# Optimization experiments

Hardware: AMD Instinct MI355X
Metric: run time of the kernel (lower is better)

Reference implementation:

```python
import jax, jax.numpy as jnp
import numpy as np

N = 100000
D_IN = 64
D_HID = 64


def _sage_conv(x, edge_index, Wl, bl, Wr):
    # PyG SAGEConv (mean aggr): out = lin_l(mean_j x_j) + lin_r(x_root)
    src, dst = edge_index[0], edge_index[1]
    n = x.shape[0]
    msg_sum = jax.ops.segment_sum(x[src], dst, num_segments=n)  # [N, d]
    deg = jax.ops.segment_sum(jnp.ones_like(src, dtype=x.dtype), dst, num_segments=n)
    agg = msg_sum / jnp.maximum(deg, 1.0)[:, None]
    return agg @ Wl + bl + x @ Wr


def setup_inputs() -> dict:
    key = jax.random.key(0)
    ks = jax.random.split(key, 8)
    x = jax.random.normal(ks[0], (N, D_IN), dtype=jnp.float32)
    edge_index = jax.random.randint(ks[1], (2, 16 * N), 0, N, dtype=jnp.int64)
    s = 1.0 / np.sqrt(D_IN)
    W1l = jax.random.uniform(ks[2], (D_IN, D_HID), minval=-s, maxval=s, dtype=jnp.float32)
    b1 = jnp.zeros((D_HID,), dtype=jnp.float32)
    W1r = jax.random.uniform(ks[3], (D_IN, D_HID), minval=-s, maxval=s, dtype=jnp.float32)
    s2 = 1.0 / np.sqrt(D_HID)
    W2l = jax.random.uniform(ks[4], (D_HID, D_HID), minval=-s2, maxval=s2, dtype=jnp.float32)
    b2 = jnp.zeros((D_HID,), dtype=jnp.float32)
    W2r = jax.random.uniform(ks[5], (D_HID, D_HID), minval=-s2, maxval=s2, dtype=jnp.float32)
    Wc = jax.random.uniform(ks[6], (D_HID, 2), minval=-s2, maxval=s2, dtype=jnp.float32)
    bc = jax.random.uniform(ks[7], (2,), minval=-s2, maxval=s2, dtype=jnp.float32)
    return {"x": x, "edge_index": edge_index, "W1l": W1l, "b1": b1, "W1r": W1r,
            "W2l": W2l, "b2": b2, "W2r": W2r, "Wc": Wc, "bc": bc}


def reference(x, edge_index, W1l, b1, W1r, W2l, b2, W2r, Wc, bc):
    h = jax.nn.relu(_sage_conv(x, edge_index, W1l, b1, W1r))
    h = _sage_conv(h, edge_index, W2l, b2, W2r)
    return h @ Wc + bc  # [N, 2] logits
```

## Files before the change

kernel.cpp:

```cpp
#include <hip/hip_runtime.h>


#define SCAN_BS 1024
#define BUCKET_BITS 9
#define BUCKET_NODES 512
#define NBUCK_MAX 256
#define EPB 8192
#define STAGE_CAP 10240

__global__ void __launch_bounds__(256) bucket_hist_kernel(const int* __restrict__ dst,
                                                          int* __restrict__ counts,
                                                          int ne, int B, int NB) {
  __shared__ int hist[NBUCK_MAX];
  for (int k = threadIdx.x; k < B; k += 256) hist[k] = 0;
  __syncthreads();
  int base = blockIdx.x * EPB;
#pragma unroll 4
  for (int i = 0; i < EPB / 256; ++i) {
    int e = base + i * 256 + threadIdx.x;
    if (e < ne) atomicAdd(&hist[dst[e] >> BUCKET_BITS], 1);
  }
  __syncthreads();
  for (int k = threadIdx.x; k < B; k += 256) counts[k * NB + blockIdx.x] = hist[k];
}

__device__ __forceinline__ int block_scan_inclusive_1024(int v, int* wsums) {
  int lane = threadIdx.x & 63;
  int wid = threadIdx.x >> 6;
  int s = v;
#pragma unroll
  for (int off = 1; off < 64; off <<= 1) {
    int t = __shfl_up(s, off);
    if (lane >= off) s += t;
  }
  if (lane == 63) wsums[wid] = s;
  __syncthreads();
  if (wid == 0) {
    int ws = (lane < 16) ? wsums[lane] : 0;
#pragma unroll
    for (int off = 1; off < 16; off <<= 1) {
      int t = __shfl_up(ws, off);
      if (lane >= off) ws += t;
    }
    if (lane < 16) wsums[lane] = ws;
  }
  __syncthreads();
  if (wid > 0) s += wsums[wid - 1];
  return s;
}

__device__ __forceinline__ int block_scan_inclusive_256(int v, int* wsums4) {
  int lane = threadIdx.x & 63;
  int wid = threadIdx.x >> 6;
  int s = v;
#pragma unroll
  for (int off = 1; off < 64; off <<= 1) {
    int t = __shfl_up(s, off);
    if (lane >= off) s += t;
  }
  if (lane == 63) wsums4[wid] = s;
  __syncthreads();
  if (wid == 0) {
    int ws = (lane < 4) ? wsums4[lane] : 0;
#pragma unroll
    for (int off = 1; off < 4; off <<= 1) {
      int t = __shfl_up(ws, off);
      if (lane >= off) ws += t;
    }
    if (lane < 4) wsums4[lane] = ws;
  }
  __syncthreads();
  if (wid > 0) s += wsums4[wid - 1];
  return s;
}

__global__ void __launch_bounds__(SCAN_BS) scan_a_inplace_kernel(int* __restrict__ data,
                                                                 int* __restrict__ bsums,
                                                                 int S) {
  __shared__ int wsums[16];
  int i = blockIdx.x * SCAN_BS + threadIdx.x;
  int v = (i < S) ? data[i] : 0;
  int inc = block_scan_inclusive_1024(v, wsums);
  if (i < S) data[i] = inc - v;
  if (threadIdx.x == SCAN_BS - 1) bsums[blockIdx.x] = inc;
}

__global__ void __launch_bounds__(SCAN_BS) scan_b_kernel(const int* __restrict__ bsums,
                                                         int* __restrict__ boffs, int nb) {
  __shared__ int wsums[16];
  int v = ((int)threadIdx.x < nb) ? bsums[threadIdx.x] : 0;
  int inc = block_scan_inclusive_1024(v, wsums);
  if ((int)threadIdx.x < nb) boffs[threadIdx.x] = inc - v;
  if ((int)threadIdx.x == nb - 1) boffs[nb] = inc;
}

__global__ void add_offs_kernel(int* __restrict__ v, const int* __restrict__ boffs, int S) {
  int i = blockIdx.x * blockDim.x + threadIdx.x;
  if (i < S) v[i] += boffs[i >> 10];
}

__global__ void __launch_bounds__(256) bucket_place_kernel(const int* __restrict__ src,
                                                           const int* __restrict__ dst,
                                                           const int* __restrict__ counts,
                                                           int* __restrict__ arr,
                                                           int ne, int B, int NB) {
  __shared__ int cur[NBUCK_MAX];
  for (int k = threadIdx.x; k < B; k += 256) cur[k] = counts[k * NB + blockIdx.x];
  __syncthreads();
  int base = blockIdx.x * EPB;
#pragma unroll 4
  for (int i = 0; i < EPB / 256; ++i) {
    int e = base + i * 256 + threadIdx.x;
    if (e < ne) {
      int d = dst[e];
      int k = d >> BUCKET_BITS;
      int pos = atomicAdd(&cur[k], 1);
      arr[pos] = (src[e] << BUCKET_BITS) | (d & (BUCKET_NODES - 1));
    }
  }
}

__global__ void __launch_bounds__(256) csr_bucket_kernel(const int* __restrict__ arr,
                                                         const int* __restrict__ counts,
                                                         int* __restrict__ row_ptr,
                                                         int* __restrict__ col,
                                                         int n, int ne, int B, int NB) {
  __shared__ int hist[BUCKET_NODES];
  __shared__ int cur[BUCKET_NODES];
  __shared__ int stage[STAGE_CAP];
  __shared__ int wsums4[4];
  int k = blockIdx.x;
  int tid = threadIdx.x;
  int start = counts[k * NB];
  int end = (k + 1 < B) ? counts[(k + 1) * NB] : ne;
  int size = end - start;
  hist[tid] = 0;
  hist[tid + 256] = 0;
  __syncthreads();
  for (int e = start + tid; e < end; e += 256)
    atomicAdd(&hist[arr[e] & (BUCKET_NODES - 1)], 1);
  __syncthreads();
  int v0 = hist[tid * 2], v1 = hist[tid * 2 + 1];
  int inc = block_scan_inclusive_256(v0 + v1, wsums4);
  int e0 = inc - (v0 + v1);
  {
    int node0 = k * BUCKET_NODES;
    cur[tid * 2] = e0;
    cur[tid * 2 + 1] = e0 + v0;
    if (node0 + tid * 2 < n) row_ptr[node0 + tid * 2] = start + e0;
    if (node0 + tid * 2 + 1 < n) row_ptr[node0 + tid * 2 + 1] = start + e0 + v0;
  }
  if (k == B - 1 && tid == 0) row_ptr[n] = ne;
  __syncthreads();
  for (int e = start + tid; e < end; e += 256) {
    int p = arr[e];
    int pos = atomicAdd(&cur[p & (BUCKET_NODES - 1)], 1);
    int s = p >> BUCKET_BITS;
    if (pos < STAGE_CAP) stage[pos] = s;
    else col[start + pos] = s;
  }
  __syncthreads();
  int lim = (size < STAGE_CAP) ? size : STAGE_CAP;
  for (int i = tid; i < lim; i += 256) col[start + i] = stage[i];
}

__global__ void __launch_bounds__(256) aggregate_kernel(const float* __restrict__ xin,
                                                        const int* __restrict__ row_ptr,
                                                        const int* __restrict__ col,
                                                        float* __restrict__ outp, int n) {
  int gwave = (blockIdx.x * 256 + threadIdx.x) >> 6;
  int lane = threadIdx.x & 63;
  if (gwave >= n) return;
  int m = __builtin_amdgcn_readfirstlane(gwave);
  int start = row_ptr[m];
  int end = row_ptr[m + 1];
  float a[16];
#pragma unroll
  for (int i = 0; i < 16; ++i) a[i] = 0.f;
  int e = start;
  for (; e + 16 <= end; e += 16) {
    int c[16];
#pragma unroll
    for (int i = 0; i < 16; ++i) c[i] = col[e + i];
#pragma unroll
    for (int i = 0; i < 16; ++i) a[i] += xin[(size_t)c[i] * 64 + lane];
  }
  for (; e + 4 <= end; e += 4) {
    int c0 = col[e + 0], c1 = col[e + 1], c2 = col[e + 2], c3 = col[e + 3];
    a[0] += xin[(size_t)c0 * 64 + lane];
    a[1] += xin[(size_t)c1 * 64 + lane];
    a[2] += xin[(size_t)c2 * 64 + lane];
    a[3] += xin[(size_t)c3 * 64 + lane];
  }
  for (; e < end; ++e) a[0] += xin[(size_t)col[e] * 64 + lane];
#pragma unroll
  for (int i = 8; i > 0; i >>= 1)
#pragma unroll
    for (int j = 0; j < i; ++j) a[j] += a[j + i];
  int d = end - start;
  float inv = 1.0f / (float)((d > 0) ? d : 1);
  outp[(size_t)m * 64 + lane] = a[0] * inv;
}

#define GBM 128

__device__ __forceinline__ void gemm_phase(const float* __restrict__ M,
                                           const float* __restrict__ W,
                                           float (&Mt)[GBM][65], float (&Ws)[64][64],
                                           float4 (&acc)[8],
                                           int node0, int n, int tx, int ty, int t) {
  __syncthreads();
#pragma unroll
  for (int i = 0; i < 8; ++i) {
    int f4 = i * 256 + t;
    int r = f4 >> 4, c4 = f4 & 15;
    int nd = node0 + r;
    float4 v = make_float4(0.f, 0.f, 0.f, 0.f);
    if (nd < n) v = ((const float4*)(M + (size_t)nd * 64))[c4];
    Mt[r][c4 * 4 + 0] = v.x; Mt[r][c4 * 4 + 1] = v.y;
    Mt[r][c4 * 4 + 2] = v.z; Mt[r][c4 * 4 + 3] = v.w;
  }
#pragma unroll
  for (int i = 0; i < 4; ++i) {
    int f4 = i * 256 + t;
    int k = f4 >> 4, c4 = f4 & 15;
    float4 v = ((const float4*)W)[f4];
    *(float4*)&Ws[k][c4 * 4] = v;
  }
  __syncthreads();
#pragma unroll 4
  for (int k = 0; k < 64; ++k) {
    float4 w4 = *(const float4*)&Ws[k][tx * 4];
    float a[8];
#pragma unroll
    for (int m = 0; m < 8; ++m) a[m] = Mt[ty * 8 + m][k];
#pragma unroll
    for (int m = 0; m < 8; ++m) {
      acc[m].x = fmaf(a[m], w4.x, acc[m].x);
      acc[m].y = fmaf(a[m], w4.y, acc[m].y);
      acc[m].z = fmaf(a[m], w4.z, acc[m].z);
      acc[m].w = fmaf(a[m], w4.w, acc[m].w);
    }
  }
}

__global__ void __launch_bounds__(256) gemm_relu_kernel(const float* __restrict__ A,
                                                        const float* __restrict__ X,
                                                        const float* __restrict__ Wl,
                                                        const float* __restrict__ bias,
                                                        const float* __restrict__ Wr,
                                                        float* __restrict__ H, int n) {
  __shared__ float Mt[GBM][65];
  __shared__ float Ws[64][64];
  int t = threadIdx.x;
  int tx = t & 15, ty = t >> 4;
  int node0 = blockIdx.x * GBM;
  float4 bv = *(const float4*)(bias + tx * 4);
  float4 acc[8];
#pragma unroll
  for (int m = 0; m < 8; ++m) acc[m] = bv;
  gemm_phase(A, Wl, Mt, Ws, acc, node0, n, tx, ty, t);
  gemm_phase(X, Wr, Mt, Ws, acc, node0, n, tx, ty, t);
#pragma unroll
  for (int m = 0; m < 8; ++m) {
    int nd = node0 + ty * 8 + m;
    if (nd < n) {
      float4 v;
      v.x = fmaxf(acc[m].x, 0.f);
      v.y = fmaxf(acc[m].y, 0.f);
      v.z = fmaxf(acc[m].z, 0.f);
      v.w = fmaxf(acc[m].w, 0.f);
      ((float4*)(H + (size_t)nd * 64))[tx] = v;
    }
  }
}

__global__ void __launch_bounds__(256) gemm_cls_kernel(const float* __restrict__ A,
                                                       const float* __restrict__ X,
                                                       const float* __restrict__ Wl,
                                                       const float* __restrict__ bias,
                                                       const float* __restrict__ Wr,
                                                       const float* __restrict__ Wc,
                                                       const float* __restrict__ bc,
                                                       float* __restrict__ outp, int n) {
  __shared__ float Mt[GBM][65];
  __shared__ float Ws[64][64];
  int t = threadIdx.x;
  int tx = t & 15, ty = t >> 4;
  int node0 = blockIdx.x * GBM;
  float4 bv = *(const float4*)(bias + tx * 4);
  float4 acc[8];
#pragma unroll
  for (int m = 0; m < 8; ++m) acc[m] = bv;
  gemm_phase(A, Wl, Mt, Ws, acc, node0, n, tx, ty, t);
  gemm_phase(X, Wr, Mt, Ws, acc, node0, n, tx, ty, t);
  float2 wc0 = *(const float2*)(Wc + (tx * 4 + 0) * 2);
  float2 wc1 = *(const float2*)(Wc + (tx * 4 + 1) * 2);
  float2 wc2 = *(const float2*)(Wc + (tx * 4 + 2) * 2);
  float2 wc3 = *(const float2*)(Wc + (tx * 4 + 3) * 2);
  float b0 = bc[0], b1 = bc[1];
#pragma unroll
  for (int m = 0; m < 8; ++m) {
    float p0 = acc[m].x * wc0.x + acc[m].y * wc1.x + acc[m].z * wc2.x + acc[m].w * wc3.x;
    float p1 = acc[m].x * wc0.y + acc[m].y * wc1.y + acc[m].z * wc2.y + acc[m].w * wc3.y;
#pragma unroll
    for (int off = 1; off < 16; off <<= 1) {
      p0 += __shfl_xor(p0, off);
      p1 += __shfl_xor(p1, off);
    }
    if (tx == 0) {
      int nd = node0 + ty * 8 + m;
      if (nd < n) {
        float2 o;
        o.x = p0 + b0;
        o.y = p1 + b1;
        *(float2*)(outp + (size_t)nd * 2) = o;
      }
    }
  }
}

extern "C" void kernel_launch(void* const* d_in, const int* in_sizes, int n_in,
                              void* d_out, int out_size, void* d_ws, size_t ws_size,
                              hipStream_t stream) {
  const float* x   = (const float*)d_in[0];
  const int*   ei  = (const int*)d_in[1];
  const float* W1l = (const float*)d_in[2];
  const float* b1  = (const float*)d_in[3];
  const float* W1r = (const float*)d_in[4];
  const float* W2l = (const float*)d_in[5];
  const float* b2  = (const float*)d_in[6];
  const float* W2r = (const float*)d_in[7];
  const float* Wc  = (const float*)d_in[8];
  const float* bc  = (const float*)d_in[9];
  float* out = (float*)d_out;

  const int n  = in_sizes[0] / 64;
  const int ne = in_sizes[1] / 2;
  const int* src = ei;
  const int* dst = ei + ne;

  const int B  = (n + BUCKET_NODES - 1) >> BUCKET_BITS;
  const int NB = (ne + EPB - 1) / EPB;
  const int S  = B * NB;
  const int nsb = (S + SCAN_BS - 1) / SCAN_BS;

  char* ws = (char*)d_ws;
  size_t off = 0;
  auto carve = [&](size_t bytes) -> void* {
    void* p = ws + off;
    off += (bytes + 255) & ~(size_t)255;
    return p;
  };
  int* counts  = (int*)carve((size_t)S * 4);
  int* bsums   = (int*)carve((size_t)(nsb + 1) * 4);
  int* boffs   = (int*)carve((size_t)(nsb + 1) * 4);
  int* col     = (int*)carve((size_t)ne * 4);
  int* row_ptr = (int*)carve((size_t)(n + 1) * 4);
  float* m1    = (float*)carve((size_t)n * 64 * 4);
  float* h     = (float*)carve((size_t)n * 64 * 4);
  int* arr     = (int*)m1;
  (void)ws_size;

  bucket_hist_kernel<<<NB, 256, 0, stream>>>(dst, counts, ne, B, NB);
  scan_a_inplace_kernel<<<nsb, SCAN_BS, 0, stream>>>(counts, bsums, S);
  scan_b_kernel<<<1, SCAN_BS, 0, stream>>>(bsums, boffs, nsb);
  add_offs_kernel<<<(S + 255) / 256, 256, 0, stream>>>(counts, boffs, S);
  bucket_place_kernel<<<NB, 256, 0, stream>>>(src, dst, counts, arr, ne, B, NB);
  csr_bucket_kernel<<<B, 256, 0, stream>>>(arr, counts, row_ptr, col, n, ne, B, NB);

  const int gtiles = (n + GBM - 1) / GBM;
  aggregate_kernel<<<(n * 64 + 255) / 256, 256, 0, stream>>>(x, row_ptr, col, m1, n);
  gemm_relu_kernel<<<gtiles, 256, 0, stream>>>(m1, x, W1l, b1, W1r, h, n);

  aggregate_kernel<<<(n * 64 + 255) / 256, 256, 0, stream>>>(h, row_ptr, col, m1, n);
  gemm_cls_kernel<<<gtiles, 256, 0, stream>>>(m1, h, W2l, b2, W2r, Wc, bc, out, n);
}
```

Baseline: 329.7 us.

## Fuse neighbor aggregation into SAGE GEMM kernels and fold scan offsets

```diff
diff --git a/kernel.cpp b/kernel.cpp
--- a/kernel.cpp
+++ b/kernel.cpp
@@ -94,18 +94,17 @@
   if ((int)threadIdx.x == nb - 1) boffs[nb] = inc;
 }
 
-__global__ void add_offs_kernel(int* __restrict__ v, const int* __restrict__ boffs, int S) {
-  int i = blockIdx.x * blockDim.x + threadIdx.x;
-  if (i < S) v[i] += boffs[i >> 10];
-}
-
 __global__ void __launch_bounds__(256) bucket_place_kernel(const int* __restrict__ src,
                                                            const int* __restrict__ dst,
                                                            const int* __restrict__ counts,
+                                                           const int* __restrict__ boffs,
                                                            int* __restrict__ arr,
                                                            int ne, int B, int NB) {
   __shared__ int cur[NBUCK_MAX];
-  for (int k = threadIdx.x; k < B; k += 256) cur[k] = counts[k * NB + blockIdx.x];
+  for (int k = threadIdx.x; k < B; k += 256) {
+    int idx = k * NB + blockIdx.x;
+    cur[k] = counts[idx] + boffs[idx >> 10];
+  }
   __syncthreads();
   int base = blockIdx.x * EPB;
 #pragma unroll 4
@@ -122,6 +121,7 @@
 
 __global__ void __launch_bounds__(256) csr_bucket_kernel(const int* __restrict__ arr,
                                                          const int* __restrict__ counts,
+                                                         const int* __restrict__ boffs,
                                                          int* __restrict__ row_ptr,
                                                          int* __restrict__ col,
                                                          int n, int ne, int B, int NB) {
@@ -131,8 +131,15 @@
   __shared__ int wsums4[4];
   int k = blockIdx.x;
   int tid = threadIdx.x;
-  int start = counts[k * NB];
-  int end = (k + 1 < B) ? counts[(k + 1) * NB] : ne;
+  int i0 = k * NB;
+  int start = counts[i0] + boffs[i0 >> 10];
+  int end;
+  if (k + 1 < B) {
+    int i1 = (k + 1) * NB;
+    end = counts[i1] + boffs[i1 >> 10];
+  } else {
+    end = ne;
+  }
   int size = end - start;
   hist[tid] = 0;
   hist[tid + 256] = 0;
@@ -164,106 +171,129 @@
   for (int i = tid; i < lim; i += 256) col[start + i] = stage[i];
 }
 
-__global__ void __launch_bounds__(256) aggregate_kernel(const float* __restrict__ xin,
-                                                        const int* __restrict__ row_ptr,
-                                                        const int* __restrict__ col,
-                                                        float* __restrict__ outp, int n) {
-  int gwave = (blockIdx.x * 256 + threadIdx.x) >> 6;
-  int lane = threadIdx.x & 63;
-  if (gwave >= n) return;
-  int m = __builtin_amdgcn_readfirstlane(gwave);
-  int start = row_ptr[m];
-  int end = row_ptr[m + 1];
-  float a[16];
-#pragma unroll
-  for (int i = 0; i < 16; ++i) a[i] = 0.f;
-  int e = start;
-  for (; e + 16 <= end; e += 16) {
-    int c[16];
-#pragma unroll
-    for (int i = 0; i < 16; ++i) c[i] = col[e + i];
-#pragma unroll
-    for (int i = 0; i < 16; ++i) a[i] += xin[(size_t)c[i] * 64 + lane];
-  }
-  for (; e + 4 <= end; e += 4) {
-    int c0 = col[e + 0], c1 = col[e + 1], c2 = col[e + 2], c3 = col[e + 3];
-    a[0] += xin[(size_t)c0 * 64 + lane];
-    a[1] += xin[(size_t)c1 * 64 + lane];
-    a[2] += xin[(size_t)c2 * 64 + lane];
-    a[3] += xin[(size_t)c3 * 64 + lane];
-  }
-  for (; e < end; ++e) a[0] += xin[(size_t)col[e] * 64 + lane];
-#pragma unroll
-  for (int i = 8; i > 0; i >>= 1)
-#pragma unroll
-    for (int j = 0; j < i; ++j) a[j] += a[j + i];
-  int d = end - start;
-  float inv = 1.0f / (float)((d > 0) ? d : 1);
-  outp[(size_t)m * 64 + lane] = a[0] * inv;
-}
-
-#define GBM 128
-
-__device__ __forceinline__ void gemm_phase(const float* __restrict__ M,
-                                           const float* __restrict__ W,
-                                           float (&Mt)[GBM][65], float (&Ws)[64][64],
-                                           float4 (&acc)[8],
-                                           int node0, int n, int tx, int ty, int t) {
-  __syncthreads();
-#pragma unroll
-  for (int i = 0; i < 8; ++i) {
-    int f4 = i * 256 + t;
+
+#define FBM 128
+#define FTHREADS 512
+
+__device__ __forceinline__ void fused_agg_phase(const float* __restrict__ X,
+                                                const int* __restrict__ row_ptr,
+                                                const int* __restrict__ col,
+                                                float (&Mt)[FBM][65],
+                                                int node0, int n, int w, int lane) {
+  for (int i = 0; i < 16; ++i) {
+    int row = w * 16 + i;
+    int m = node0 + row;
+    float mean = 0.f;
+    if (m < n) {
+      int start = row_ptr[m];
+      int end = row_ptr[m + 1];
+      float a[16];
+#pragma unroll
+      for (int j = 0; j < 16; ++j) a[j] = 0.f;
+      int e = start;
+      for (; e + 16 <= end; e += 16) {
+        int c[16];
+#pragma unroll
+        for (int j = 0; j < 16; ++j) c[j] = col[e + j];
+#pragma unroll
+        for (int j = 0; j < 16; ++j) a[j] += X[(size_t)c[j] * 64 + lane];
+      }
+      for (; e < end; ++e) a[0] += X[(size_t)col[e] * 64 + lane];
+#pragma unroll
+      for (int s = 8; s > 0; s >>= 1)
+#pragma unroll
+        for (int j = 0; j < s; ++j) a[j] += a[j + s];
+      int d = end - start;
+      mean = a[0] / (float)((d > 0) ? d : 1);
+    }
+    Mt[row][lane] = mean;
+  }
+}
+
+__device__ __forceinline__ void fused_gemm_accum(float (&Mt)[FBM][65],
+                                                 float (&Ws)[64][64],
+                                                 float4 (&acc)[4], int tx, int ty) {
+#pragma unroll 4
+  for (int k = 0; k < 64; ++k) {
+    float4 w4 = *(const float4*)&Ws[k][tx * 4];
+    float a0 = Mt[ty * 4 + 0][k];
+    float a1 = Mt[ty * 4 + 1][k];
+    float a2 = Mt[ty * 4 + 2][k];
+    float a3 = Mt[ty * 4 + 3][k];
+    acc[0].x = fmaf(a0, w4.x, acc[0].x);
+    acc[0].y = fmaf(a0, w4.y, acc[0].y);
+    acc[0].z = fmaf(a0, w4.z, acc[0].z);
+    acc[0].w = fmaf(a0, w4.w, acc[0].w);
+    acc[1].x = fmaf(a1, w4.x, acc[1].x);
+    acc[1].y = fmaf(a1, w4.y, acc[1].y);
+    acc[1].z = fmaf(a1, w4.z, acc[1].z);
+    acc[1].w = fmaf(a1, w4.w, acc[1].w);
+    acc[2].x = fmaf(a2, w4.x, acc[2].x);
+    acc[2].y = fmaf(a2, w4.y, acc[2].y);
+    acc[2].z = fmaf(a2, w4.z, acc[2].z);
+    acc[2].w = fmaf(a2, w4.w, acc[2].w);
+    acc[3].x = fmaf(a3, w4.x, acc[3].x);
+    acc[3].y = fmaf(a3, w4.y, acc[3].y);
+    acc[3].z = fmaf(a3, w4.z, acc[3].z);
+    acc[3].w = fmaf(a3, w4.w, acc[3].w);
+  }
+}
+
+__device__ __forceinline__ void fused_stage_w(const float* __restrict__ W,
+                                              float (&Ws)[64][64], int t) {
+#pragma unroll
+  for (int i = 0; i < 2; ++i) {
+    int f4 = i * FTHREADS + t;
+    int k = f4 >> 4, c4 = f4 & 15;
+    *(float4*)&Ws[k][c4 * 4] = ((const float4*)W)[f4];
+  }
+}
+
+__device__ __forceinline__ void fused_stage_x(const float* __restrict__ X,
+                                              float (&Mt)[FBM][65],
+                                              int node0, int n, int t) {
+#pragma unroll
+  for (int i = 0; i < 4; ++i) {
+    int f4 = i * FTHREADS + t;
     int r = f4 >> 4, c4 = f4 & 15;
     int nd = node0 + r;
     float4 v = make_float4(0.f, 0.f, 0.f, 0.f);
-    if (nd < n) v = ((const float4*)(M + (size_t)nd * 64))[c4];
-    Mt[r][c4 * 4 + 0] = v.x; Mt[r][c4 * 4 + 1] = v.y;
-    Mt[r][c4 * 4 + 2] = v.z; Mt[r][c4 * 4 + 3] = v.w;
-  }
-#pragma unroll
-  for (int i = 0; i < 4; ++i) {
-    int f4 = i * 256 + t;
-    int k = f4 >> 4, c4 = f4 & 15;
-    float4 v = ((const float4*)W)[f4];
-    *(float4*)&Ws[k][c4 * 4] = v;
-  }
-  __syncthreads();
-#pragma unroll 4
-  for (int k = 0; k < 64; ++k) {
-    float4 w4 = *(const float4*)&Ws[k][tx * 4];
-    float a[8];
-#pragma unroll
-    for (int m = 0; m < 8; ++m) a[m] = Mt[ty * 8 + m][k];
-#pragma unroll
-    for (int m = 0; m < 8; ++m) {
-      acc[m].x = fmaf(a[m], w4.x, acc[m].x);
-      acc[m].y = fmaf(a[m], w4.y, acc[m].y);
-      acc[m].z = fmaf(a[m], w4.z, acc[m].z);
-      acc[m].w = fmaf(a[m], w4.w, acc[m].w);
-    }
-  }
-}
-
-__global__ void __launch_bounds__(256) gemm_relu_kernel(const float* __restrict__ A,
-                                                        const float* __restrict__ X,
-                                                        const float* __restrict__ Wl,
-                                                        const float* __restrict__ bias,
-                                                        const float* __restrict__ Wr,
-                                                        float* __restrict__ H, int n) {
-  __shared__ float Mt[GBM][65];
+    if (nd < n) v = ((const float4*)(X + (size_t)nd * 64))[c4];
+    Mt[r][c4 * 4 + 0] = v.x;
+    Mt[r][c4 * 4 + 1] = v.y;
+    Mt[r][c4 * 4 + 2] = v.z;
+    Mt[r][c4 * 4 + 3] = v.w;
+  }
+}
+
+__global__ void __launch_bounds__(FTHREADS) agg_gemm_relu_kernel(
+    const float* __restrict__ X, const int* __restrict__ row_ptr,
+    const int* __restrict__ col, const float* __restrict__ Wl,
+    const float* __restrict__ bias, const float* __restrict__ Wr,
+    float* __restrict__ H, int n) {
+  __shared__ float Mt[FBM][65];
   __shared__ float Ws[64][64];
   int t = threadIdx.x;
+  int lane = t & 63;
+  int w = __builtin_amdgcn_readfirstlane(t >> 6);
+  int node0 = blockIdx.x * FBM;
+  fused_agg_phase(X, row_ptr, col, Mt, node0, n, w, lane);
+  fused_stage_w(Wl, Ws, t);
+  __syncthreads();
   int tx = t & 15, ty = t >> 4;
-  int node0 = blockIdx.x * GBM;
   float4 bv = *(const float4*)(bias + tx * 4);
-  float4 acc[8];
-#pragma unroll
-  for (int m = 0; m < 8; ++m) acc[m] = bv;
-  gemm_phase(A, Wl, Mt, Ws, acc, node0, n, tx, ty, t);
-  gemm_phase(X, Wr, Mt, Ws, acc, node0, n, tx, ty, t);
-#pragma unroll
-  for (int m = 0; m < 8; ++m) {
-    int nd = node0 + ty * 8 + m;
+  float4 acc[4];
+#pragma unroll
+  for (int m = 0; m < 4; ++m) acc[m] = bv;
+  fused_gemm_accum(Mt, Ws, acc, tx, ty);
+  __syncthreads();
+  fused_stage_x(X, Mt, node0, n, t);
+  fused_stage_w(Wr, Ws, t);
+  __syncthreads();
+  fused_gemm_accum(Mt, Ws, acc, tx, ty);
+#pragma unroll
+  for (int m = 0; m < 4; ++m) {
+    int nd = node0 + ty * 4 + m;
     if (nd < n) {
       float4 v;
       v.x = fmaxf(acc[m].x, 0.f);
@@ -275,32 +305,39 @@
   }
 }
 
-__global__ void __launch_bounds__(256) gemm_cls_kernel(const float* __restrict__ A,
-                                                       const float* __restrict__ X,
-                                                       const float* __restrict__ Wl,
-                                                       const float* __restrict__ bias,
-                                                       const float* __restrict__ Wr,
-                                                       const float* __restrict__ Wc,
-                                                       const float* __restrict__ bc,
-                                                       float* __restrict__ outp, int n) {
-  __shared__ float Mt[GBM][65];
+__global__ void __launch_bounds__(FTHREADS) agg_gemm_cls_kernel(
+    const float* __restrict__ X, const int* __restrict__ row_ptr,
+    const int* __restrict__ col, const float* __restrict__ Wl,
+    const float* __restrict__ bias, const float* __restrict__ Wr,
+    const float* __restrict__ Wc, const float* __restrict__ bc,
+    float* __restrict__ outp, int n) {
+  __shared__ float Mt[FBM][65];
   __shared__ float Ws[64][64];
   int t = threadIdx.x;
+  int lane = t & 63;
+  int w = __builtin_amdgcn_readfirstlane(t >> 6);
+  int node0 = blockIdx.x * FBM;
+  fused_agg_phase(X, row_ptr, col, Mt, node0, n, w, lane);
+  fused_stage_w(Wl, Ws, t);
+  __syncthreads();
   int tx = t & 15, ty = t >> 4;
-  int node0 = blockIdx.x * GBM;
   float4 bv = *(const float4*)(bias + tx * 4);
-  float4 acc[8];
-#pragma unroll
-  for (int m = 0; m < 8; ++m) acc[m] = bv;
-  gemm_phase(A, Wl, Mt, Ws, acc, node0, n, tx, ty, t);
-  gemm_phase(X, Wr, Mt, Ws, acc, node0, n, tx, ty, t);
+  float4 acc[4];
+#pragma unroll
+  for (int m = 0; m < 4; ++m) acc[m] = bv;
+  fused_gemm_accum(Mt, Ws, acc, tx, ty);
+  __syncthreads();
+  fused_stage_x(X, Mt, node0, n, t);
+  fused_stage_w(Wr, Ws, t);
+  __syncthreads();
+  fused_gemm_accum(Mt, Ws, acc, tx, ty);
   float2 wc0 = *(const float2*)(Wc + (tx * 4 + 0) * 2);
   float2 wc1 = *(const float2*)(Wc + (tx * 4 + 1) * 2);
   float2 wc2 = *(const float2*)(Wc + (tx * 4 + 2) * 2);
   float2 wc3 = *(const float2*)(Wc + (tx * 4 + 3) * 2);
   float b0 = bc[0], b1 = bc[1];
 #pragma unroll
-  for (int m = 0; m < 8; ++m) {
+  for (int m = 0; m < 4; ++m) {
     float p0 = acc[m].x * wc0.x + acc[m].y * wc1.x + acc[m].z * wc2.x + acc[m].w * wc3.x;
     float p1 = acc[m].x * wc0.y + acc[m].y * wc1.y + acc[m].z * wc2.y + acc[m].w * wc3.y;
 #pragma unroll
@@ -309,7 +346,7 @@
       p1 += __shfl_xor(p1, off);
     }
     if (tx == 0) {
-      int nd = node0 + ty * 8 + m;
+      int nd = node0 + ty * 4 + m;
       if (nd < n) {
         float2 o;
         o.x = p0 + b0;
@@ -357,22 +394,17 @@
   int* boffs   = (int*)carve((size_t)(nsb + 1) * 4);
   int* col     = (int*)carve((size_t)ne * 4);
   int* row_ptr = (int*)carve((size_t)(n + 1) * 4);
-  float* m1    = (float*)carve((size_t)n * 64 * 4);
+  int* arr     = (int*)carve((size_t)ne * 4);
   float* h     = (float*)carve((size_t)n * 64 * 4);
-  int* arr     = (int*)m1;
   (void)ws_size;
 
   bucket_hist_kernel<<<NB, 256, 0, stream>>>(dst, counts, ne, B, NB);
   scan_a_inplace_kernel<<<nsb, SCAN_BS, 0, stream>>>(counts, bsums, S);
   scan_b_kernel<<<1, SCAN_BS, 0, stream>>>(bsums, boffs, nsb);
-  add_offs_kernel<<<(S + 255) / 256, 256, 0, stream>>>(counts, boffs, S);
-  bucket_place_kernel<<<NB, 256, 0, stream>>>(src, dst, counts, arr, ne, B, NB);
-  csr_bucket_kernel<<<B, 256, 0, stream>>>(arr, counts, row_ptr, col, n, ne, B, NB);
-
-  const int gtiles = (n + GBM - 1) / GBM;
-  aggregate_kernel<<<(n * 64 + 255) / 256, 256, 0, stream>>>(x, row_ptr, col, m1, n);
-  gemm_relu_kernel<<<gtiles, 256, 0, stream>>>(m1, x, W1l, b1, W1r, h, n);
-
-  aggregate_kernel<<<(n * 64 + 255) / 256, 256, 0, stream>>>(h, row_ptr, col, m1, n);
-  gemm_cls_kernel<<<gtiles, 256, 0, stream>>>(m1, h, W2l, b2, W2r, Wc, bc, out, n);
-}
+  bucket_place_kernel<<<NB, 256, 0, stream>>>(src, dst, counts, boffs, arr, ne, B, NB);
+  csr_bucket_kernel<<<B, 256, 0, stream>>>(arr, counts, boffs, row_ptr, col, n, ne, B, NB);
+
+  const int ftiles = (n + FBM - 1) / FBM;
+  agg_gemm_relu_kernel<<<ftiles, FTHREADS, 0, stream>>>(x, row_ptr, col, W1l, b1, W1r, h, n);
+  agg_gemm_cls_kernel<<<ftiles, FTHREADS, 0, stream>>>(h, row_ptr, col, W2l, b2, W2r, Wc, bc, out, n);
+}
```

New measurement: 400.8 us. +21.5%, slower.
